# Optimization experiments

Measured on AMD Instinct MI355X. Metric: run time of the kernel, lower is better.

Reference implementation:

```python
import jax, jax.numpy as jnp
import numpy as np

N_SAMPLES = 8388608  # total packed samples across all rays
N_RAYS = 131072      # number of rays (segments)


def setup_inputs() -> dict:
    key = jax.random.key(0)
    k1, k2, k3 = jax.random.split(key, 3)
    # Sorted segment ids emulate the packed ray layout (samples of a ray are contiguous).
    segment_ids = jnp.sort(
        jax.random.randint(k1, (N_SAMPLES,), 0, N_RAYS, dtype=jnp.int32)
    )
    rgb_samples = jax.random.normal(k2, (N_SAMPLES, 3), dtype=jnp.float32)
    weights_samples = jax.random.uniform(k3, (N_SAMPLES, 1), dtype=jnp.float32)
    return {
        "segment_ids": segment_ids,
        "rgb_samples": rgb_samples,
        "weights_samples": weights_samples,
        "n_rays": N_RAYS,
    }


def reference(segment_ids, rgb_samples, weights_samples, n_rays):
    # pred_rgb[r] = sum over samples s belonging to ray r of w_s * rgb_s
    weighted = rgb_samples * weights_samples  # [N,3], weight broadcast over channels
    pred_rgb = jax.ops.segment_sum(weighted, segment_ids, num_segments=n_rays)  # [n_rays,3]
    return pred_rgb
```

## Files before the change

### kernel.cpp

```cpp
#include <hip/hip_runtime.h>


#define NTHREADS 256

__global__ __launch_bounds__(NTHREADS) void zero_out_kernel(float4* __restrict__ out4,
                                                            int n4) {
  int i = blockIdx.x * blockDim.x + threadIdx.x;
  if (i < n4) out4[i] = make_float4(0.f, 0.f, 0.f, 0.f);
}

__global__ __launch_bounds__(NTHREADS) void integrate_kernel(
    const int* __restrict__ ids, const float* __restrict__ rgb,
    const float* __restrict__ w, float* __restrict__ out, int n_samples) {
  const int lane = threadIdx.x & 63;
  const long long t0 = (long long)(blockIdx.x * blockDim.x + threadIdx.x) * 4;

  int idv[4];
  float px[4], py[4], pz[4];
  if (t0 + 3 < n_samples) {
    const int4   id4 = *(const int4*)(ids + t0);
    const float4 w4  = *(const float4*)(w + t0);
    const float4 r0  = *(const float4*)(rgb + 3 * t0);
    const float4 r1  = *(const float4*)(rgb + 3 * t0 + 4);
    const float4 r2  = *(const float4*)(rgb + 3 * t0 + 8);
    idv[0] = id4.x; idv[1] = id4.y; idv[2] = id4.z; idv[3] = id4.w;
    px[0] = r0.x * w4.x; py[0] = r0.y * w4.x; pz[0] = r0.z * w4.x;
    px[1] = r0.w * w4.y; py[1] = r1.x * w4.y; pz[1] = r1.y * w4.y;
    px[2] = r1.z * w4.z; py[2] = r1.w * w4.z; pz[2] = r2.x * w4.z;
    px[3] = r2.y * w4.w; py[3] = r2.z * w4.w; pz[3] = r2.w * w4.w;
  } else {
    int last = ids[n_samples - 1];
    #pragma unroll
    for (int j = 0; j < 4; ++j) {
      long long s = t0 + j;
      if (s < n_samples) {
        idv[j] = ids[s];
        float ww = w[s];
        px[j] = rgb[3 * s + 0] * ww;
        py[j] = rgb[3 * s + 1] * ww;
        pz[j] = rgb[3 * s + 2] * ww;
      } else {
        idv[j] = (j == 0) ? last : idv[j - 1];
        px[j] = py[j] = pz[j] = 0.f;
      }
    }
  }

  const int id0 = idv[0], id3 = idv[3];
  const bool f_intra = (id0 != id3);
  const int hl = (idv[1] == id0) ? ((idv[2] == id0) ? ((idv[3] == id0) ? 4 : 3) : 2) : 1;
  const int tl = (idv[2] == id3) ? ((idv[1] == id3) ? ((idv[0] == id3) ? 4 : 3) : 2) : 1;
  float hx = 0.f, hy = 0.f, hz = 0.f, tx = 0.f, ty = 0.f, tz = 0.f;
  #pragma unroll
  for (int j = 0; j < 4; ++j) {
    if (j < hl)     { hx += px[j]; hy += py[j]; hz += pz[j]; }
    if (j >= 4 - tl){ tx += px[j]; ty += py[j]; tz += pz[j]; }
  }
  {
    int ilo = hl, ihi = 3 - tl;
    if (ilo <= ihi) {
      if (ilo == ihi) {
        atomicAdd(&out[3 * idv[ilo] + 0], px[ilo]);
        atomicAdd(&out[3 * idv[ilo] + 1], py[ilo]);
        atomicAdd(&out[3 * idv[ilo] + 2], pz[ilo]);
      } else if (idv[ilo] == idv[ihi]) {
        atomicAdd(&out[3 * idv[ilo] + 0], px[ilo] + px[ihi]);
        atomicAdd(&out[3 * idv[ilo] + 1], py[ilo] + py[ihi]);
        atomicAdd(&out[3 * idv[ilo] + 2], pz[ilo] + pz[ihi]);
      } else {
        atomicAdd(&out[3 * idv[ilo] + 0], px[ilo]);
        atomicAdd(&out[3 * idv[ilo] + 1], py[ilo]);
        atomicAdd(&out[3 * idv[ilo] + 2], pz[ilo]);
        atomicAdd(&out[3 * idv[ihi] + 0], px[ihi]);
        atomicAdd(&out[3 * idv[ihi] + 1], py[ihi]);
        atomicAdd(&out[3 * idv[ihi] + 2], pz[ihi]);
      }
    }
  }

  const int prev_tid = __shfl_up(id3, 1, 64);
  int fl = (lane == 0 || f_intra || prev_tid != id0) ? 1 : 0;
  float sx = tx, sy = ty, sz = tz;
  #pragma unroll
  for (int off = 1; off < 64; off <<= 1) {
    float ox = __shfl_up(sx, off, 64);
    float oy = __shfl_up(sy, off, 64);
    float oz = __shfl_up(sz, off, 64);
    int  ofl = __shfl_up(fl, off, 64);
    if (lane >= off && fl == 0) { sx += ox; sy += oy; sz += oz; fl = ofl; }
  }

  const float pSx = __shfl_up(sx, 1, 64);
  const float pSy = __shfl_up(sy, 1, 64);
  const float pSz = __shfl_up(sz, 1, 64);
  if (f_intra) {
    const bool link = (lane > 0) && (prev_tid == id0);
    atomicAdd(&out[3 * id0 + 0], hx + (link ? pSx : 0.f));
    atomicAdd(&out[3 * id0 + 1], hy + (link ? pSy : 0.f));
    atomicAdd(&out[3 * id0 + 2], hz + (link ? pSz : 0.f));
  }

  const int next_hid = __shfl_down(id0, 1, 64);
  if (lane == 63 || next_hid != id3) {
    atomicAdd(&out[3 * id3 + 0], sx);
    atomicAdd(&out[3 * id3 + 1], sy);
    atomicAdd(&out[3 * id3 + 2], sz);
  }
}

extern "C" void kernel_launch(void* const* d_in, const int* in_sizes, int n_in,
                              void* d_out, int out_size, void* d_ws, size_t ws_size,
                              hipStream_t stream) {
  const int*   segment_ids = (const int*)d_in[0];
  const float* rgb         = (const float*)d_in[1];
  const float* weights     = (const float*)d_in[2];
  float*       out         = (float*)d_out;

  const int n_samples = in_sizes[0];

  {
    int n4 = out_size / 4;
    int blocks = (n4 + NTHREADS - 1) / NTHREADS;
    zero_out_kernel<<<blocks, NTHREADS, 0, stream>>>((float4*)out, n4);
  }
  {
    int spb = NTHREADS * 4;
    int blocks = (n_samples + spb - 1) / spb;
    integrate_kernel<<<blocks, NTHREADS, 0, stream>>>(
        segment_ids, rgb, weights, out, n_samples);
  }
}
```

Before: 194.8 us.

## Process sixteen samples per thread with sequential run-length accumulation

Each thread now loads sixteen contiguous samples instead of four and reduces them with a sequential run scan, issuing atomics only for interior runs. The wave-level segmented scan is unchanged but handles four times fewer boundary values. This cuts atomic traffic and shuffle work per sample. In exchange, per-thread loads become strided across lanes, which can hurt coalescing, and register pressure rises.

```diff
diff --git a/kernel.cpp b/kernel.cpp
--- a/kernel.cpp
+++ b/kernel.cpp
@@ -2,6 +2,7 @@
 
 
 #define NTHREADS 256
+#define SPT 16
 
 __global__ __launch_bounds__(NTHREADS) void zero_out_kernel(float4* __restrict__ out4,
                                                             int n4) {
@@ -13,32 +14,48 @@
     const int* __restrict__ ids, const float* __restrict__ rgb,
     const float* __restrict__ w, float* __restrict__ out, int n_samples) {
   const int lane = threadIdx.x & 63;
-  const long long t0 = (long long)(blockIdx.x * blockDim.x + threadIdx.x) * 4;
+  const long long base = (long long)(blockIdx.x * blockDim.x + threadIdx.x) * SPT;
 
-  int idv[4];
-  float px[4], py[4], pz[4];
-  if (t0 + 3 < n_samples) {
-    const int4   id4 = *(const int4*)(ids + t0);
-    const float4 w4  = *(const float4*)(w + t0);
-    const float4 r0  = *(const float4*)(rgb + 3 * t0);
-    const float4 r1  = *(const float4*)(rgb + 3 * t0 + 4);
-    const float4 r2  = *(const float4*)(rgb + 3 * t0 + 8);
-    idv[0] = id4.x; idv[1] = id4.y; idv[2] = id4.z; idv[3] = id4.w;
-    px[0] = r0.x * w4.x; py[0] = r0.y * w4.x; pz[0] = r0.z * w4.x;
-    px[1] = r0.w * w4.y; py[1] = r1.x * w4.y; pz[1] = r1.y * w4.y;
-    px[2] = r1.z * w4.z; py[2] = r1.w * w4.z; pz[2] = r2.x * w4.z;
-    px[3] = r2.y * w4.w; py[3] = r2.z * w4.w; pz[3] = r2.w * w4.w;
+  int idv[SPT];
+  float px[SPT], py[SPT], pz[SPT];
+
+  if (base + (SPT - 1) < (long long)n_samples) {
+    float ww[SPT], rr[3 * SPT];
+    #pragma unroll
+    for (int b = 0; b < SPT / 4; ++b) {
+      const int4 t = *(const int4*)(ids + base + 4 * b);
+      idv[4 * b + 0] = t.x; idv[4 * b + 1] = t.y;
+      idv[4 * b + 2] = t.z; idv[4 * b + 3] = t.w;
+    }
+    #pragma unroll
+    for (int b = 0; b < SPT / 4; ++b) {
+      const float4 t = *(const float4*)(w + base + 4 * b);
+      ww[4 * b + 0] = t.x; ww[4 * b + 1] = t.y;
+      ww[4 * b + 2] = t.z; ww[4 * b + 3] = t.w;
+    }
+    #pragma unroll
+    for (int m = 0; m < 3 * SPT / 4; ++m) {
+      const float4 t = *(const float4*)(rgb + 3 * base + 4 * m);
+      rr[4 * m + 0] = t.x; rr[4 * m + 1] = t.y;
+      rr[4 * m + 2] = t.z; rr[4 * m + 3] = t.w;
+    }
+    #pragma unroll
+    for (int k = 0; k < SPT; ++k) {
+      px[k] = rr[3 * k + 0] * ww[k];
+      py[k] = rr[3 * k + 1] * ww[k];
+      pz[k] = rr[3 * k + 2] * ww[k];
+    }
   } else {
-    int last = ids[n_samples - 1];
+    const int last = ids[n_samples - 1];
     #pragma unroll
-    for (int j = 0; j < 4; ++j) {
-      long long s = t0 + j;
+    for (int j = 0; j < SPT; ++j) {
+      const long long s = base + j;
       if (s < n_samples) {
         idv[j] = ids[s];
-        float ww = w[s];
-        px[j] = rgb[3 * s + 0] * ww;
-        py[j] = rgb[3 * s + 1] * ww;
-        pz[j] = rgb[3 * s + 2] * ww;
+        const float t = w[s];
+        px[j] = rgb[3 * s + 0] * t;
+        py[j] = rgb[3 * s + 1] * t;
+        pz[j] = rgb[3 * s + 2] * t;
       } else {
         idv[j] = (j == 0) ? last : idv[j - 1];
         px[j] = py[j] = pz[j] = 0.f;
@@ -46,47 +63,38 @@
     }
   }
 
-  const int id0 = idv[0], id3 = idv[3];
-  const bool f_intra = (id0 != id3);
-  const int hl = (idv[1] == id0) ? ((idv[2] == id0) ? ((idv[3] == id0) ? 4 : 3) : 2) : 1;
-  const int tl = (idv[2] == id3) ? ((idv[1] == id3) ? ((idv[0] == id3) ? 4 : 3) : 2) : 1;
-  float hx = 0.f, hy = 0.f, hz = 0.f, tx = 0.f, ty = 0.f, tz = 0.f;
+  const int first_id = idv[0];
+  int run_id = first_id;
+  float rx = px[0], ry = py[0], rz = pz[0];
+  float hx = 0.f, hy = 0.f, hz = 0.f;
+  bool f_intra = false;
   #pragma unroll
-  for (int j = 0; j < 4; ++j) {
-    if (j < hl)     { hx += px[j]; hy += py[j]; hz += pz[j]; }
-    if (j >= 4 - tl){ tx += px[j]; ty += py[j]; tz += pz[j]; }
-  }
-  {
-    int ilo = hl, ihi = 3 - tl;
-    if (ilo <= ihi) {
-      if (ilo == ihi) {
-        atomicAdd(&out[3 * idv[ilo] + 0], px[ilo]);
-        atomicAdd(&out[3 * idv[ilo] + 1], py[ilo]);
-        atomicAdd(&out[3 * idv[ilo] + 2], pz[ilo]);
-      } else if (idv[ilo] == idv[ihi]) {
-        atomicAdd(&out[3 * idv[ilo] + 0], px[ilo] + px[ihi]);
-        atomicAdd(&out[3 * idv[ilo] + 1], py[ilo] + py[ihi]);
-        atomicAdd(&out[3 * idv[ilo] + 2], pz[ilo] + pz[ihi]);
+  for (int k = 1; k < SPT; ++k) {
+    if (idv[k] == run_id) {
+      rx += px[k]; ry += py[k]; rz += pz[k];
+    } else {
+      if (!f_intra) {
+        hx = rx; hy = ry; hz = rz; f_intra = true;
       } else {
-        atomicAdd(&out[3 * idv[ilo] + 0], px[ilo]);
-        atomicAdd(&out[3 * idv[ilo] + 1], py[ilo]);
-        atomicAdd(&out[3 * idv[ilo] + 2], pz[ilo]);
-        atomicAdd(&out[3 * idv[ihi] + 0], px[ihi]);
-        atomicAdd(&out[3 * idv[ihi] + 1], py[ihi]);
-        atomicAdd(&out[3 * idv[ihi] + 2], pz[ihi]);
+        atomicAdd(&out[3 * run_id + 0], rx);
+        atomicAdd(&out[3 * run_id + 1], ry);
+        atomicAdd(&out[3 * run_id + 2], rz);
       }
+      run_id = idv[k];
+      rx = px[k]; ry = py[k]; rz = pz[k];
     }
   }
+  const int last_id = run_id;
 
-  const int prev_tid = __shfl_up(id3, 1, 64);
-  int fl = (lane == 0 || f_intra || prev_tid != id0) ? 1 : 0;
-  float sx = tx, sy = ty, sz = tz;
+  const int prev_tid = __shfl_up(last_id, 1, 64);
+  int fl = (lane == 0 || f_intra || prev_tid != first_id) ? 1 : 0;
+  float sx = rx, sy = ry, sz = rz;
   #pragma unroll
   for (int off = 1; off < 64; off <<= 1) {
-    float ox = __shfl_up(sx, off, 64);
-    float oy = __shfl_up(sy, off, 64);
-    float oz = __shfl_up(sz, off, 64);
-    int  ofl = __shfl_up(fl, off, 64);
+    const float ox = __shfl_up(sx, off, 64);
+    const float oy = __shfl_up(sy, off, 64);
+    const float oz = __shfl_up(sz, off, 64);
+    const int ofl = __shfl_up(fl, off, 64);
     if (lane >= off && fl == 0) { sx += ox; sy += oy; sz += oz; fl = ofl; }
   }
 
@@ -94,17 +102,17 @@
   const float pSy = __shfl_up(sy, 1, 64);
   const float pSz = __shfl_up(sz, 1, 64);
   if (f_intra) {
-    const bool link = (lane > 0) && (prev_tid == id0);
-    atomicAdd(&out[3 * id0 + 0], hx + (link ? pSx : 0.f));
-    atomicAdd(&out[3 * id0 + 1], hy + (link ? pSy : 0.f));
-    atomicAdd(&out[3 * id0 + 2], hz + (link ? pSz : 0.f));
+    const bool link = (lane > 0) && (prev_tid == first_id);
+    atomicAdd(&out[3 * first_id + 0], hx + (link ? pSx : 0.f));
+    atomicAdd(&out[3 * first_id + 1], hy + (link ? pSy : 0.f));
+    atomicAdd(&out[3 * first_id + 2], hz + (link ? pSz : 0.f));
   }
 
-  const int next_hid = __shfl_down(id0, 1, 64);
-  if (lane == 63 || next_hid != id3) {
-    atomicAdd(&out[3 * id3 + 0], sx);
-    atomicAdd(&out[3 * id3 + 1], sy);
-    atomicAdd(&out[3 * id3 + 2], sz);
+  const int next_hid = __shfl_down(first_id, 1, 64);
+  if (lane == 63 || next_hid != last_id) {
+    atomicAdd(&out[3 * last_id + 0], sx);
+    atomicAdd(&out[3 * last_id + 1], sy);
+    atomicAdd(&out[3 * last_id + 2], sz);
   }
 }
 
@@ -124,7 +132,7 @@
     zero_out_kernel<<<blocks, NTHREADS, 0, stream>>>((float4*)out, n4);
   }
   {
-    int spb = NTHREADS * 4;
+    int spb = NTHREADS * SPT;
     int blocks = (n_samples + spb - 1) / spb;
     integrate_kernel<<<blocks, NTHREADS, 0, stream>>>(
         segment_ids, rgb, weights, out, n_samples);
```

New measurement: 195.9 us. About the same (+0.6%).
